# Kernel optimization log

Hardware: AMD Instinct MI355X
Metric: run time of the kernel (lower is better)

## Reference

```python
import jax, jax.numpy as jnp
import numpy as np
import math

HIDDEN = 1024
N_HEADS = 16
HEAD = HIDDEN // N_HEADS

def setup_inputs() -> dict:
    key = jax.random.key(0)
    k1, k2, k3 = jax.random.split(key, 3)
    encodings = jax.random.normal(k1, (2, 2048, HIDDEN), dtype=jnp.float32)
    W_attn = jax.random.normal(k2, (HIDDEN, 3 * HIDDEN), dtype=jnp.float32) * 0.02
    b_attn = jnp.zeros((3 * HIDDEN,), dtype=jnp.float32)
    W_out = jax.random.normal(k3, (HIDDEN, HIDDEN), dtype=jnp.float32) * 0.02
    b_out = jnp.zeros((HIDDEN,), dtype=jnp.float32)
    return {"encodings": encodings, "W_attn": W_attn, "b_attn": b_attn,
            "W_out": W_out, "b_out": b_out}

def reference(encodings, W_attn, b_attn, W_out, b_out):
    b, n, _ = encodings.shape
    qkv = encodings @ W_attn + b_attn              # [b, n, 3*hidden]
    q, k, v = jnp.split(qkv, 3, axis=-1)
    # 'b n (h l) -> b h n l'
    def to_heads(t):
        return t.reshape(b, n, N_HEADS, HEAD).transpose(0, 2, 1, 3)
    q, k, v = to_heads(q), to_heads(k), to_heads(v)
    # scores[b,h,k,q]; causal mask keeps key_pos <= query_pos
    scores = jnp.einsum('bhki,bhqi->bhkq', k, q) / math.sqrt(HEAD)
    mask = jnp.arange(n)[:, None] <= jnp.arange(n)[None, :]   # [k, q]
    scores = jnp.where(mask, scores, jnp.float32(-10000.0))
    attn = jax.nn.softmax(scores, axis=2)          # softmax over key dim
    combined = jnp.einsum('bhkq,bhkl->bhql', attn, v)  # [b, h, n, head]
    out = combined.transpose(0, 2, 1, 3).reshape(b, n, HIDDEN)
    return out @ W_out + b_out
```

## Files before the change

kernel.cpp:

```cpp
#include <hip/hip_runtime.h>
#include <hip/hip_bf16.h>

typedef __attribute__((ext_vector_type(8))) short bf16x8;
typedef __attribute__((ext_vector_type(4))) short bf16x4;
typedef __attribute__((ext_vector_type(4))) float f32x4;

__device__ __forceinline__ short f2bf(float f) {
    unsigned u = __float_as_uint(f);
    u += 0x7fff + ((u >> 16) & 1);
    return (short)(u >> 16);
}
__device__ __forceinline__ float bf2f(short s) {
    return __uint_as_float(((unsigned)(unsigned short)s) << 16);
}
__device__ __forceinline__ unsigned pk_bf16(float lo, float hi) {
    __hip_bfloat162 t = __float22bfloat162_rn(make_float2(lo, hi));
    unsigned u;
    __builtin_memcpy(&u, &t, 4);
    return u;
}

#define GLOAD_LDS16(gp, lp)                                                            \
    __builtin_amdgcn_global_load_lds(                                                  \
        (const __attribute__((address_space(1))) unsigned*)(gp),                       \
        (__attribute__((address_space(3))) unsigned*)(lp), 16, 0, 0)

#define QK_SCALE 0.180336879f
#define MFMA16(a, b, c) __builtin_amdgcn_mfma_f32_16x16x32_bf16((a), (b), (c), 0, 0, 0)

__device__ __forceinline__ void tcvt_tile(const float* __restrict__ W, short* __restrict__ Wt,
                                          int K, int N, int bx, int by, int t,
                                          short (*tile)[72]) {
    const int k0 = by * 64, n0 = bx * 64;
    #pragma unroll
    for (int jj = 0; jj < 4; ++jj) {
        int row = jj * 16 + (t >> 4);
        int col = (t & 15) * 4;
        f32x4 v = *(const f32x4*)&W[(size_t)(k0 + row) * N + n0 + col];
        bf16x4 b = {f2bf(v.x), f2bf(v.y), f2bf(v.z), f2bf(v.w)};
        *(bf16x4*)&tile[row][col] = b;
    }
    __syncthreads();
    const int nr = t >> 2, kc = (t & 3) * 16;
    bf16x8 o0, o1;
    #pragma unroll
    for (int j = 0; j < 8; ++j) { o0[j] = tile[kc + j][nr]; o1[j] = tile[kc + 8 + j][nr]; }
    short* dst = &Wt[(size_t)(n0 + nr) * K + k0 + kc];
    *(bf16x8*)dst = o0;
    *(bf16x8*)(dst + 8) = o1;
}

__global__ __launch_bounds__(256) void prep_kernel(
    const float* __restrict__ enc, const float* __restrict__ Wa,
    const float* __restrict__ ba, const float* __restrict__ Wo,
    const float* __restrict__ bo, short* __restrict__ Abf,
    short* __restrict__ WtA, short* __restrict__ bbA,
    short* __restrict__ WtO, short* __restrict__ bbO)
{
    __shared__ alignas(16) short tile[64][72];
    const int id = blockIdx.x, t = threadIdx.x;
    if (id < 2048) {
        const int i = id * 2048 + t * 8;
        f32x4 a = *(const f32x4*)&enc[i];
        f32x4 b = *(const f32x4*)&enc[i + 4];
        bf16x8 o = {f2bf(a.x), f2bf(a.y), f2bf(a.z), f2bf(a.w),
                    f2bf(b.x), f2bf(b.y), f2bf(b.z), f2bf(b.w)};
        *(bf16x8*)&Abf[i] = o;
    } else if (id == 2048) {
        for (int j = t * 8; j < 3072; j += 2048) {
            f32x4 a = *(const f32x4*)&ba[j];
            f32x4 b = *(const f32x4*)&ba[j + 4];
            bf16x8 o = {f2bf(a.x), f2bf(a.y), f2bf(a.z), f2bf(a.w),
                        f2bf(b.x), f2bf(b.y), f2bf(b.z), f2bf(b.w)};
            *(bf16x8*)&bbA[j] = o;
        }
    } else if (id == 2049) {
        if (t < 128) {
            const int j = t * 8;
            f32x4 a = *(const f32x4*)&bo[j];
            f32x4 b = *(const f32x4*)&bo[j + 4];
            bf16x8 o = {f2bf(a.x), f2bf(a.y), f2bf(a.z), f2bf(a.w),
                        f2bf(b.x), f2bf(b.y), f2bf(b.z), f2bf(b.w)};
            *(bf16x8*)&bbO[j] = o;
        }
        __syncthreads();
    } else if (id < 2818) {
        const int lid = id - 2050;
        tcvt_tile(Wa, WtA, 1024, 3072, lid % 48, lid / 48, t, tile);
    } else {
        const int lid = id - 2818;
        tcvt_tile(Wo, WtO, 1024, 1024, lid % 16, lid / 16, t, tile);
    }
}

template<int BN, bool F32OUT, bool SPLIT3>
__global__ __launch_bounds__(256) void gemm_bt(
    const short* __restrict__ A, const short* __restrict__ Bt,
    const short* __restrict__ bias, void* __restrict__ C,
    short* __restrict__ Kw, short* __restrict__ Vw, int M, int N, int K)
{
    __shared__ alignas(16) short LB[2][128 * 64 + BN * 64];
    short* Ct = &LB[0][0];

    const int tid = threadIdx.x, w = tid >> 6, lane = tid & 63;
    const int quad = lane >> 4, l16 = lane & 15;
    constexpr int MT = (BN == 128) ? 4 : 2;
    const int wm = (BN == 128) ? (w >> 1) : w;
    const int wn = (BN == 128) ? (w & 1) : 0;
    const int m0 = blockIdx.y * 128, n0 = blockIdx.x * BN;
    const int srow = lane >> 3;
    const int scol = ((lane & 7) ^ srow) * 8;

    f32x4 acc[MT][4] = {};

    #define STAGE_G(k0s, buf)                                                               \
        do {                                                                                \
            short* As_ = &LB[buf][0];                                                       \
            short* Bs_ = &LB[buf][128 * 64];                                                \
            _Pragma("unroll")                                                               \
            for (int jj = 0; jj < 4; ++jj) {                                                \
                const int rb = w * 32 + jj * 8;                                             \
                GLOAD_LDS16(&A[(size_t)(m0 + rb + srow) * K + (k0s) + scol], &As_[rb * 64]);\
            }                                                                               \
            if (BN == 128) {                                                                \
                _Pragma("unroll")                                                           \
                for (int jj = 0; jj < 4; ++jj) {                                            \
                    const int rb = w * 32 + jj * 8;                                         \
                    GLOAD_LDS16(&Bt[(size_t)(n0 + rb + srow) * K + (k0s) + scol],           \
                                &Bs_[rb * 64]);                                             \
                }                                                                           \
            } else {                                                                        \
                _Pragma("unroll")                                                           \
                for (int jj = 0; jj < 2; ++jj) {                                            \
                    const int rb = w * 16 + jj * 8;                                         \
                    GLOAD_LDS16(&Bt[(size_t)(n0 + rb + srow) * K + (k0s) + scol],           \
                                &Bs_[rb * 64]);                                             \
                }                                                                           \
            }                                                                               \
        } while (0)

    STAGE_G(0, 0);

    int cur = 0;
    for (int k0 = 0; k0 < K; k0 += 64) {
        const int kn = (k0 + 64 < K) ? k0 + 64 : k0;
        STAGE_G(kn, cur ^ 1);

        if (BN == 128) asm volatile("s_waitcnt vmcnt(8)" ::: "memory");
        else           asm volatile("s_waitcnt vmcnt(6)" ::: "memory");
        __builtin_amdgcn_s_barrier();
        __builtin_amdgcn_sched_barrier(0);

        const short* As = &LB[cur][0];
        const short* Bs = &LB[cur][128 * 64];
        #pragma unroll
        for (int half = 0; half < 2; ++half) {
            const int kc2 = half * 4 + quad;
            bf16x8 af[MT], bfr[4];
            #pragma unroll
            for (int i = 0; i < MT; ++i) {
                const int row = wm * (MT * 16) + i * 16 + l16;
                af[i] = *(const bf16x8*)&As[row * 64 + ((kc2 ^ (row & 7)) << 3)];
            }
            #pragma unroll
            for (int i = 0; i < 4; ++i) {
                const int row = wn * 64 + i * 16 + l16;
                bfr[i] = *(const bf16x8*)&Bs[row * 64 + ((kc2 ^ (row & 7)) << 3)];
            }
            __builtin_amdgcn_s_setprio(1);
            #pragma unroll
            for (int mt = 0; mt < MT; ++mt)
                #pragma unroll
                for (int nt = 0; nt < 4; ++nt)
                    acc[mt][nt] = MFMA16(af[mt], bfr[nt], acc[mt][nt]);
            __builtin_amdgcn_s_setprio(0);
        }

        __builtin_amdgcn_s_barrier();
        cur ^= 1;
    }
    #undef STAGE_G

    asm volatile("s_waitcnt vmcnt(0)" ::: "memory");
    __builtin_amdgcn_s_barrier();

    if (SPLIT3) {
        const int g = n0 >> 10;
        const int lc0 = n0 & 1023;
        if (g < 2) {
            #pragma unroll
            for (int nt = 0; nt < 4; ++nt) {
                const int col = wn * 64 + nt * 16 + l16;
                const float bv = bf2f(bias[n0 + col]);
                const int chunk = col >> 3, wi = col & 7;
                #pragma unroll
                for (int mt = 0; mt < 4; ++mt) {
                    const int rbase = wm * 64 + mt * 16 + quad * 4;
                    #pragma unroll
                    for (int r = 0; r < 4; ++r) {
                        const int row = rbase + r;
                        float v = acc[mt][nt][r] + bv;
                        if (g == 0) v *= QK_SCALE;
                        Ct[row * 128 + (((chunk ^ (row & 15)) << 3) | wi)] = f2bf(v);
                    }
                }
            }
        } else {
            #pragma unroll
            for (int nt = 0; nt < 4; ++nt) {
                const int d = wn * 64 + nt * 16 + l16;
                const float bv = bf2f(bias[n0 + d]);
                const int dsw = d & 15;
                #pragma unroll
                for (int mt = 0; mt < 4; ++mt) {
                    const int key0 = wm * 64 + mt * 16 + quad * 4;
                    bf16x4 p = {f2bf(acc[mt][nt][0] + bv), f2bf(acc[mt][nt][1] + bv),
                                f2bf(acc[mt][nt][2] + bv), f2bf(acc[mt][nt][3] + bv)};
                    *(bf16x4*)&Ct[d * 128 + ((((key0 >> 3) ^ dsw) << 3) | (key0 & 7))] = p;
                }
            }
        }
        __syncthreads();
        const int batch = m0 >> 11;
        const int kc0 = (m0 & 2047) >> 6;
        const int head0 = lc0 >> 6;
        if (g == 0) {
            short* dst = (short*)C;
            #pragma unroll
            for (int i = 0; i < 8; ++i) {
                const int idx = i * 256 + tid;
                const int row = idx >> 4, chunk = idx & 15;
                bf16x8 v = *(const bf16x8*)&Ct[row * 128 + ((chunk ^ (row & 15)) << 3)];
                *(bf16x8*)&dst[(size_t)(m0 + row) * 1024 + lc0 + chunk * 8] = v;
            }
        } else if (g == 1) {
            #pragma unroll
            for (int i = 0; i < 8; ++i) {
                const int idx = i * 256 + tid;
                const int qd = idx >> 9, c = idx & 511;
                const int kcL = qd >> 1, headL = qd & 1;
                const int s = c >> 7, h2 = (c >> 6) & 1;
                const int l16c = c & 15, quadc = (c >> 4) & 3;
                const int row = kcL * 64 + s * 16 + l16c;
                const int colc = headL * 8 + h2 * 4 + quadc;
                bf16x8 v = *(const bf16x8*)&Ct[row * 128 + ((colc ^ (row & 15)) << 3)];
                const int bh = batch * 16 + head0 + headL, kc = kc0 + kcL;
                *(bf16x8*)&Kw[((size_t)(bh * 32 + kc) * 512 + c) * 8] = v;
            }
        } else {
            #pragma unroll
            for (int i = 0; i < 8; ++i) {
                const int idx = i * 256 + tid;
                const int qd = idx >> 9, c = idx & 511;
                const int kcL = qd >> 1, headL = qd & 1;
                const int h2 = c >> 8, dt = (c >> 6) & 3;
                const int l16c = c & 15, quadc = (c >> 4) & 3;
                const int d = headL * 64 + dt * 16 + l16c;
                const int Ka = kcL * 64 + h2 * 32 + quadc * 4;
                const int Kb = Ka + 16;
                bf16x4 va = *(const bf16x4*)&Ct[d * 128 + (((Ka >> 3) ^ (d & 15)) << 3) + (Ka & 7)];
                bf16x4 vb = *(const bf16x4*)&Ct[d * 128 + (((Kb >> 3) ^ (d & 15)) << 3) + (Kb & 7)];
                bf16x8 v = {va[0], va[1], va[2], va[3], vb[0], vb[1], vb[2], vb[3]};
                const int bh = batch * 16 + head0 + headL, kc = kc0 + kcL;
                *(bf16x8*)&Vw[((size_t)(bh * 32 + kc) * 512 + c) * 8] = v;
            }
        }
    } else {
        #pragma unroll
        for (int nt = 0; nt < 4; ++nt) {
            const int col = n0 + wn * 64 + nt * 16 + l16;
            const float bv = bf2f(bias[col]);
            #pragma unroll
            for (int mt = 0; mt < MT; ++mt) {
                const int row = m0 + wm * (MT * 16) + mt * 16 + quad * 4;
                #pragma unroll
                for (int r = 0; r < 4; ++r) {
                    float v = acc[mt][nt][r] + bv;
                    if (F32OUT) ((float*)C)[(size_t)(row + r) * N + col] = v;
                    else        ((short*)C)[(size_t)(row + r) * N + col] = f2bf(v);
                }
            }
        }
    }
}

__global__ __launch_bounds__(256) void attn_kernel(
    const short* __restrict__ Qw, const short* __restrict__ Kx,
    const short* __restrict__ Vx, short* __restrict__ comb)
{
    __shared__ alignas(16) short KV[3][2][4096];

    const int tid = threadIdx.x, w4 = tid >> 6, lane = tid & 63;
    const int quad = lane >> 4, l16 = lane & 15;
    const int blk = blockIdx.x;
    const int n = 31 - (blk >> 5);
    const int bh = blk & 31;
    const int batch = bh >> 4, head = bh & 15;
    const size_t rowbase = (size_t)batch * 2048;
    const int hcol = head * 64;
    const int q0 = n * 64 + w4 * 16;
    const short* Kxbh = Kx + (size_t)bh * 131072;
    const short* Vxbh = Vx + (size_t)bh * 131072;
    const int lofs = lane * 8;

    bf16x8 qf[2];
    {
        const short* pq = &Qw[(rowbase + q0 + l16) * 1024 + hcol];
        qf[0] = *(const bf16x8*)(pq + quad * 8);
        qf[1] = *(const bf16x8*)(pq + 32 + quad * 8);
    }
    asm volatile("s_waitcnt vmcnt(0)" ::: "memory");

    f32x4 ot[4] = {};
    float lacc = 0.f;

    const int sbase = w4 * 64;

    #define STAGE_KV(kcs, buf)                                                              \
        do {                                                                                \
            const size_t nb_ = (size_t)(kcs)*4096;                                          \
            _Pragma("unroll")                                                               \
            for (int j = 0; j < 2; ++j) {                                                   \
                GLOAD_LDS16(&Kxbh[nb_ + (size_t)(j * 256 + sbase + lane) * 8],              \
                            &KV[buf][0][(j * 256 + sbase) * 8]);                            \
                GLOAD_LDS16(&Vxbh[nb_ + (size_t)(j * 256 + sbase + lane) * 8],              \
                            &KV[buf][1][(j * 256 + sbase) * 8]);                            \
            }                                                                               \
        } while (0)

    STAGE_KV(0, 0);
    STAGE_KV((n >= 1) ? 1 : 0, 1);
    asm volatile("s_waitcnt vmcnt(4)" ::: "memory");
    __builtin_amdgcn_s_barrier();
    __builtin_amdgcn_sched_barrier(0);

    int cur = 0;
    for (int kc = 0; kc <= n; ++kc) {
        {
            const int ks = (kc + 2 <= n) ? kc + 2 : n;
            const int wb = (cur + 2 >= 3) ? cur - 1 : cur + 2;
            STAGE_KV(ks, wb);
        }

        bf16x8 kf[4][2];
        #pragma unroll
        for (int s = 0; s < 4; ++s) {
            kf[s][0] = *(const bf16x8*)&KV[cur][0][(s * 2 + 0) * 512 + lofs];
            kf[s][1] = *(const bf16x8*)&KV[cur][0][(s * 2 + 1) * 512 + lofs];
        }

        f32x4 sv[4];
        __builtin_amdgcn_s_setprio(1);
        #pragma unroll
        for (int s = 0; s < 4; ++s) {
            f32x4 a = {0.f, 0.f, 0.f, 0.f};
            a = MFMA16(kf[s][0], qf[0], a);
            a = MFMA16(kf[s][1], qf[1], a);
            sv[s] = a;
        }
        __builtin_amdgcn_s_setprio(0);

        bf16x8 vf[2][4];
        #pragma unroll
        for (int hh = 0; hh < 2; ++hh)
            #pragma unroll
            for (int dt = 0; dt < 4; ++dt)
                vf[hh][dt] = *(const bf16x8*)&KV[cur][1][(hh * 4 + dt) * 512 + lofs];

        if (kc == n) {
            const int qq = q0 + l16;
            #pragma unroll
            for (int s = 0; s < 4; ++s) {
                const int keyb = kc * 64 + s * 16 + quad * 4;
                #pragma unroll
                for (int r = 0; r < 4; ++r)
                    sv[s][r] = (keyb + r <= qq) ? sv[s][r] : -1e30f;
            }
        }
        {
            unsigned u[4][2];
            #pragma unroll
            for (int s = 0; s < 4; ++s) {
                #pragma unroll
                for (int r = 0; r < 4; ++r) sv[s][r] = exp2f(sv[s][r]);
                lacc += (sv[s][0] + sv[s][1]) + (sv[s][2] + sv[s][3]);
                u[s][0] = pk_bf16(sv[s][0], sv[s][1]);
                u[s][1] = pk_bf16(sv[s][2], sv[s][3]);
            }
            bf16x8 pf0, pf1;
            {
                unsigned t0[4] = {u[0][0], u[0][1], u[1][0], u[1][1]};
                unsigned t1[4] = {u[2][0], u[2][1], u[3][0], u[3][1]};
                __builtin_memcpy(&pf0, t0, 16);
                __builtin_memcpy(&pf1, t1, 16);
            }
            __builtin_amdgcn_s_setprio(1);
            #pragma unroll
            for (int dt = 0; dt < 4; ++dt) {
                ot[dt] = MFMA16(vf[0][dt], pf0, ot[dt]);
                ot[dt] = MFMA16(vf[1][dt], pf1, ot[dt]);
            }
            __builtin_amdgcn_s_setprio(0);
        }

        asm volatile("s_waitcnt vmcnt(4)" ::: "memory");
        __builtin_amdgcn_s_barrier();
        __builtin_amdgcn_sched_barrier(0);
        cur = (cur + 1 >= 3) ? 0 : cur + 1;
    }
    #undef STAGE_KV

    asm volatile("s_waitcnt vmcnt(0)" ::: "memory");
    __builtin_amdgcn_s_barrier();

    lacc += __shfl_xor(lacc, 16);
    lacc += __shfl_xor(lacc, 32);
    const float inv = 1.0f / lacc;

    short* pw = &KV[0][0][0] + w4 * 1152;
    #pragma unroll
    for (int dt = 0; dt < 4; ++dt) {
        *(unsigned*)&pw[l16 * 72 + dt * 16 + quad * 4]     = pk_bf16(ot[dt][0] * inv, ot[dt][1] * inv);
        *(unsigned*)&pw[l16 * 72 + dt * 16 + quad * 4 + 2] = pk_bf16(ot[dt][2] * inv, ot[dt][3] * inv);
    }
    {
        const int qr = lane >> 2, dc = (lane & 3) * 16;
        bf16x8 a0 = *(const bf16x8*)&pw[qr * 72 + dc];
        bf16x8 a1 = *(const bf16x8*)&pw[qr * 72 + dc + 8];
        short* dst = &comb[(rowbase + q0 + qr) * 1024 + hcol + dc];
        *(bf16x8*)dst = a0;
        *(bf16x8*)(dst + 8) = a1;
    }
}

extern "C" void kernel_launch(void* const* d_in, const int* in_sizes, int n_in,
                              void* d_out, int out_size, void* d_ws, size_t ws_size,
                              hipStream_t stream)
{
    const float* enc = (const float*)d_in[0];
    const float* Wa  = (const float*)d_in[1];
    const float* ba  = (const float*)d_in[2];
    const float* Wo  = (const float*)d_in[3];
    const float* bo  = (const float*)d_in[4];
    float* out = (float*)d_out;

    char* ws = (char*)d_ws;
    short* Abf  = (short*)ws;
    short* comb = (short*)ws;
    short* WtO  = (short*)(ws + ((size_t)8 << 20));
    short* bbA  = (short*)(ws + ((size_t)10 << 20));
    short* bbO  = (short*)(ws + ((size_t)10 << 20) + 16384);
    short* WtA  = (short*)(ws + ((size_t)11 << 20));
    short* Kx   = (short*)(ws + ((size_t)17 << 20));
    short* Vx   = (short*)(ws + ((size_t)25 << 20));
    short* Qw   = (short*)(ws + ((size_t)33 << 20));

    prep_kernel<<<3074, 256, 0, stream>>>(enc, Wa, ba, Wo, bo, Abf, WtA, bbA, WtO, bbO);
    gemm_bt<128, false, true><<<dim3(24, 32), 256, 0, stream>>>(
        Abf, WtA, bbA, Qw, Kx, Vx, 4096, 3072, 1024);
    attn_kernel<<<1024, 256, 0, stream>>>(Qw, Kx, Vx, comb);
    gemm_bt<128, true, false><<<dim3(8, 32), 256, 0, stream>>>(
        comb, WtO, bbO, out, nullptr, nullptr, 4096, 1024, 1024);
}
```

Measured before the change: 169.6 us.

## Process 128 queries per attention block to reuse each K/V tile twice

Each attention block now covers a 128-query band, with each wave owning two 16-row query tiles instead of one. Every K/V chunk staged into LDS is therefore used for twice as many queries, which halves global/L2 K/V traffic and the staging and barrier work per query. In exchange the grid shrinks to 512 blocks, which lowers parallelism and makes the causal load imbalance coarser. On the last two key chunks some waves also compute fully masked scores, which is wasted work.

Result: slower. 183.1 us (+7.9%).

```diff
diff --git a/kernel.cpp b/kernel.cpp
--- a/kernel.cpp
+++ b/kernel.cpp
@@ -293,26 +293,28 @@
     const int tid = threadIdx.x, w4 = tid >> 6, lane = tid & 63;
     const int quad = lane >> 4, l16 = lane & 15;
     const int blk = blockIdx.x;
-    const int n = 31 - (blk >> 5);
+    const int band = 15 - (blk >> 5);
     const int bh = blk & 31;
     const int batch = bh >> 4, head = bh & 15;
     const size_t rowbase = (size_t)batch * 2048;
     const int hcol = head * 64;
-    const int q0 = n * 64 + w4 * 16;
+    const int q0 = band * 128 + w4 * 32;
+    const int maxD = 2 * band + 1;
     const short* Kxbh = Kx + (size_t)bh * 131072;
     const short* Vxbh = Vx + (size_t)bh * 131072;
     const int lofs = lane * 8;
 
-    bf16x8 qf[2];
-    {
-        const short* pq = &Qw[(rowbase + q0 + l16) * 1024 + hcol];
-        qf[0] = *(const bf16x8*)(pq + quad * 8);
-        qf[1] = *(const bf16x8*)(pq + 32 + quad * 8);
+    bf16x8 qf[2][2];
+    #pragma unroll
+    for (int t16 = 0; t16 < 2; ++t16) {
+        const short* pq = &Qw[(rowbase + q0 + t16 * 16 + l16) * 1024 + hcol];
+        qf[t16][0] = *(const bf16x8*)(pq + quad * 8);
+        qf[t16][1] = *(const bf16x8*)(pq + 32 + quad * 8);
     }
     asm volatile("s_waitcnt vmcnt(0)" ::: "memory");
 
-    f32x4 ot[4] = {};
-    float lacc = 0.f;
+    f32x4 ot[2][4] = {};
+    float lacc[2] = {0.f, 0.f};
 
     const int sbase = w4 * 64;
 
@@ -329,15 +331,15 @@
         } while (0)
 
     STAGE_KV(0, 0);
-    STAGE_KV((n >= 1) ? 1 : 0, 1);
+    STAGE_KV(1, 1);
     asm volatile("s_waitcnt vmcnt(4)" ::: "memory");
     __builtin_amdgcn_s_barrier();
     __builtin_amdgcn_sched_barrier(0);
 
     int cur = 0;
-    for (int kc = 0; kc <= n; ++kc) {
+    for (int kc = 0; kc <= maxD; ++kc) {
         {
-            const int ks = (kc + 2 <= n) ? kc + 2 : n;
+            const int ks = (kc + 2 <= maxD) ? kc + 2 : maxD;
             const int wb = (cur + 2 >= 3) ? cur - 1 : cur + 2;
             STAGE_KV(ks, wb);
         }
@@ -349,14 +351,17 @@
             kf[s][1] = *(const bf16x8*)&KV[cur][0][(s * 2 + 1) * 512 + lofs];
         }
 
-        f32x4 sv[4];
+        f32x4 sv[2][4];
         __builtin_amdgcn_s_setprio(1);
         #pragma unroll
         for (int s = 0; s < 4; ++s) {
-            f32x4 a = {0.f, 0.f, 0.f, 0.f};
-            a = MFMA16(kf[s][0], qf[0], a);
-            a = MFMA16(kf[s][1], qf[1], a);
-            sv[s] = a;
+            #pragma unroll
+            for (int t16 = 0; t16 < 2; ++t16) {
+                f32x4 a = {0.f, 0.f, 0.f, 0.f};
+                a = MFMA16(kf[s][0], qf[t16][0], a);
+                a = MFMA16(kf[s][1], qf[t16][1], a);
+                sv[t16][s] = a;
+            }
         }
         __builtin_amdgcn_s_setprio(0);
 
@@ -367,25 +372,26 @@
             for (int dt = 0; dt < 4; ++dt)
                 vf[hh][dt] = *(const bf16x8*)&KV[cur][1][(hh * 4 + dt) * 512 + lofs];
 
-        if (kc == n) {
-            const int qq = q0 + l16;
+        #pragma unroll
+        for (int t16 = 0; t16 < 2; ++t16) {
+            if (kc >= 2 * band) {
+                const int qq = q0 + t16 * 16 + l16;
+                #pragma unroll
+                for (int s = 0; s < 4; ++s) {
+                    const int keyb = kc * 64 + s * 16 + quad * 4;
+                    #pragma unroll
+                    for (int r = 0; r < 4; ++r)
+                        sv[t16][s][r] = (keyb + r <= qq) ? sv[t16][s][r] : -1e30f;
+                }
+            }
+            unsigned u[4][2];
             #pragma unroll
             for (int s = 0; s < 4; ++s) {
-                const int keyb = kc * 64 + s * 16 + quad * 4;
-                #pragma unroll
-                for (int r = 0; r < 4; ++r)
-                    sv[s][r] = (keyb + r <= qq) ? sv[s][r] : -1e30f;
-            }
-        }
-        {
-            unsigned u[4][2];
-            #pragma unroll
-            for (int s = 0; s < 4; ++s) {
-                #pragma unroll
-                for (int r = 0; r < 4; ++r) sv[s][r] = exp2f(sv[s][r]);
-                lacc += (sv[s][0] + sv[s][1]) + (sv[s][2] + sv[s][3]);
-                u[s][0] = pk_bf16(sv[s][0], sv[s][1]);
-                u[s][1] = pk_bf16(sv[s][2], sv[s][3]);
+                #pragma unroll
+                for (int r = 0; r < 4; ++r) sv[t16][s][r] = exp2f(sv[t16][s][r]);
+                lacc[t16] += (sv[t16][s][0] + sv[t16][s][1]) + (sv[t16][s][2] + sv[t16][s][3]);
+                u[s][0] = pk_bf16(sv[t16][s][0], sv[t16][s][1]);
+                u[s][1] = pk_bf16(sv[t16][s][2], sv[t16][s][3]);
             }
             bf16x8 pf0, pf1;
             {
@@ -397,8 +403,8 @@
             __builtin_amdgcn_s_setprio(1);
             #pragma unroll
             for (int dt = 0; dt < 4; ++dt) {
-                ot[dt] = MFMA16(vf[0][dt], pf0, ot[dt]);
-                ot[dt] = MFMA16(vf[1][dt], pf1, ot[dt]);
+                ot[t16][dt] = MFMA16(vf[0][dt], pf0, ot[t16][dt]);
+                ot[t16][dt] = MFMA16(vf[1][dt], pf1, ot[t16][dt]);
             }
             __builtin_amdgcn_s_setprio(0);
         }
@@ -413,21 +419,22 @@
     asm volatile("s_waitcnt vmcnt(0)" ::: "memory");
     __builtin_amdgcn_s_barrier();
 
-    lacc += __shfl_xor(lacc, 16);
-    lacc += __shfl_xor(lacc, 32);
-    const float inv = 1.0f / lacc;
-
-    short* pw = &KV[0][0][0] + w4 * 1152;
     #pragma unroll
-    for (int dt = 0; dt < 4; ++dt) {
-        *(unsigned*)&pw[l16 * 72 + dt * 16 + quad * 4]     = pk_bf16(ot[dt][0] * inv, ot[dt][1] * inv);
-        *(unsigned*)&pw[l16 * 72 + dt * 16 + quad * 4 + 2] = pk_bf16(ot[dt][2] * inv, ot[dt][3] * inv);
-    }
-    {
+    for (int t16 = 0; t16 < 2; ++t16) {
+        lacc[t16] += __shfl_xor(lacc[t16], 16);
+        lacc[t16] += __shfl_xor(lacc[t16], 32);
+        const float inv = 1.0f / lacc[t16];
+
+        short* pw = &KV[0][0][0] + (w4 * 2 + t16) * 1152;
+        #pragma unroll
+        for (int dt = 0; dt < 4; ++dt) {
+            *(unsigned*)&pw[l16 * 72 + dt * 16 + quad * 4]     = pk_bf16(ot[t16][dt][0] * inv, ot[t16][dt][1] * inv);
+            *(unsigned*)&pw[l16 * 72 + dt * 16 + quad * 4 + 2] = pk_bf16(ot[t16][dt][2] * inv, ot[t16][dt][3] * inv);
+        }
         const int qr = lane >> 2, dc = (lane & 3) * 16;
         bf16x8 a0 = *(const bf16x8*)&pw[qr * 72 + dc];
         bf16x8 a1 = *(const bf16x8*)&pw[qr * 72 + dc + 8];
-        short* dst = &comb[(rowbase + q0 + qr) * 1024 + hcol + dc];
+        short* dst = &comb[(rowbase + q0 + t16 * 16 + qr) * 1024 + hcol + dc];
         *(bf16x8*)dst = a0;
         *(bf16x8*)(dst + 8) = a1;
     }
@@ -458,7 +465,7 @@
     prep_kernel<<<3074, 256, 0, stream>>>(enc, Wa, ba, Wo, bo, Abf, WtA, bbA, WtO, bbO);
     gemm_bt<128, false, true><<<dim3(24, 32), 256, 0, stream>>>(
         Abf, WtA, bbA, Qw, Kx, Vx, 4096, 3072, 1024);
-    attn_kernel<<<1024, 256, 0, stream>>>(Qw, Kx, Vx, comb);
+    attn_kernel<<<512, 256, 0, stream>>>(Qw, Kx, Vx, comb);
     gemm_bt<128, true, false><<<dim3(8, 32), 256, 0, stream>>>(
         comb, WtO, bbO, out, nullptr, nullptr, 4096, 1024, 1024);
 }
```
